# Performance work log

Measured on AMD Instinct MI355X. Metric: run time of the kernel, lower is better.

The kernel has to match this reference:

```python
import jax, jax.numpy as jnp
import numpy as np

B, S, E = 2, 2048, 1024
H, D = 16, 64          # num_heads, head_dim
FF = 4096              # ff_dim = 4*E
EPS = 1e-5


def _layer_norm(x, g, b):
    mu = jnp.mean(x, axis=-1, keepdims=True)
    var = jnp.mean(jnp.square(x - mu), axis=-1, keepdims=True)
    return (x - mu) * jax.lax.rsqrt(var + EPS) * g + b


def setup_inputs() -> dict:
    key = jax.random.key(0)
    ks = jax.random.split(key, 9)
    s = lambda fan_in: 1.0 / np.sqrt(fan_in)
    return {
        "x": jax.random.normal(ks[0], (B, S, E), dtype=jnp.float32),
        "w_qkv": jax.random.uniform(ks[1], (3 * E, E), jnp.float32, -s(E), s(E)),
        "b_qkv": jnp.zeros((3 * E,), jnp.float32),
        "w_out": jax.random.uniform(ks[2], (E, E), jnp.float32, -s(E), s(E)),
        "b_out": jnp.zeros((E,), jnp.float32),
        "g1": jnp.ones((E,), jnp.float32),
        "beta1": jnp.zeros((E,), jnp.float32),
        "w_fc1": jax.random.uniform(ks[3], (FF, E), jnp.float32, -s(E), s(E)),
        "b_fc1": jnp.zeros((FF,), jnp.float32),
        "w_fc2": jax.random.uniform(ks[4], (E, FF), jnp.float32, -s(FF), s(FF)),
        "b_fc2": jnp.zeros((E,), jnp.float32),
        "g2": jnp.ones((E,), jnp.float32),
        "beta2": jnp.zeros((E,), jnp.float32),
    }


def reference(x, w_qkv, b_qkv, w_out, b_out, g1, beta1, w_fc1, b_fc1, w_fc2, b_fc2, g2, beta2):
    scale = 1.0 / np.sqrt(D)
    # QKV projection: [B,S,3E] -> [3,B,H,S,D]
    qkv = (x @ w_qkv.T + b_qkv).reshape(B, S, 3, H, D).transpose(2, 0, 3, 1, 4)
    q, k, v = qkv[0], qkv[1], qkv[2]
    attn = jax.nn.softmax(jnp.einsum('bhqd,bhkd->bhqk', q, k) * scale, axis=-1)
    out = jnp.einsum('bhqk,bhkd->bhqd', attn, v)          # [B,H,S,D]
    out = out.transpose(0, 2, 1, 3).reshape(B, S, E)
    attn_out = out @ w_out.T + b_out
    x1 = _layer_norm(x + attn_out, g1, beta1)
    h = jax.nn.gelu(x1 @ w_fc1.T + b_fc1, approximate=False)  # torch GELU = exact erf
    ff_out = h @ w_fc2.T + b_fc2
    return _layer_norm(x1 + ff_out, g2, beta2)
```

## Files before the change

kernel.cpp:

```cpp
#include <hip/hip_runtime.h>
#include <hip/hip_bf16.h>
#include <math.h>
#include <type_traits>

typedef __hip_bfloat16 bf16;
using short8  = __attribute__((ext_vector_type(8))) short;
using short4v = __attribute__((ext_vector_type(4))) short;
using f32x4   = __attribute__((ext_vector_type(4))) float;

#define TS 2048
#define TH 16
#define TD 64
#define TE 1024
#define T2E 2048

__device__ __forceinline__ void gload16(void* lds, const void* g) {
    __builtin_amdgcn_global_load_lds(
        (__attribute__((address_space(1))) void*)g,
        (__attribute__((address_space(3))) void*)lds, 16, 0, 0);
}

__device__ __forceinline__ uint32_t pktrunc(float a, float b) {
    return (__builtin_bit_cast(uint32_t, a) >> 16) |
           (__builtin_bit_cast(uint32_t, b) & 0xFFFF0000u);
}

__global__ __launch_bounds__(256) void f2b_multi(
    const float* __restrict__ s0, bf16* __restrict__ d0,
    const float* __restrict__ s1, bf16* __restrict__ d1,
    const float* __restrict__ s2, bf16* __restrict__ d2,
    const float* __restrict__ s3, bf16* __restrict__ d3,
    const float* __restrict__ s4, bf16* __restrict__ d4)
{
    int blk = blockIdx.x;
    const float* s; bf16* d; int base;
    if (blk < 2048)      { s = s0; d = d0; base = 0; }
    else if (blk < 3584) { s = s1; d = d1; base = 2048; }
    else if (blk < 4096) { s = s2; d = d2; base = 3584; }
    else if (blk < 6144) { s = s3; d = d3; base = 4096; }
    else                 { s = s4; d = d4; base = 6144; }
    size_t i = ((size_t)(blk - base) * 256 + threadIdx.x) * 8;
    float4 a = *(const float4*)&s[i];
    float4 b = *(const float4*)&s[i + 4];
    bf16 t[8];
    t[0] = __float2bfloat16(a.x); t[1] = __float2bfloat16(a.y);
    t[2] = __float2bfloat16(a.z); t[3] = __float2bfloat16(a.w);
    t[4] = __float2bfloat16(b.x); t[5] = __float2bfloat16(b.y);
    t[6] = __float2bfloat16(b.z); t[7] = __float2bfloat16(b.w);
    *(uint4*)&d[i] = *(uint4*)t;
}

template <typename TC, bool GELU, bool QS, bool WVT, int BN>
__global__ __launch_bounds__(512, 2) void gemm256(
    const bf16* __restrict__ A, const bf16* __restrict__ Bw,
    const float* __restrict__ bias, TC* __restrict__ C,
    bf16* __restrict__ vTout, int M, int N, int K, int kLen, int Cstride)
{
    constexpr int NB = BN / 64;
    constexpr int NI = BN / 64;
    constexpr int WN = BN / 4;
    __shared__ bf16 As[2][256 * 64];
    __shared__ bf16 Bs[2][BN * 64];

    const int t    = threadIdx.x;
    const int lane = t & 63;
    const int wv   = t >> 6;
    const int wr   = wv >> 2;
    const int wc   = wv & 3;
    const int lr   = lane & 15;
    const int lq   = lane >> 4;

    const int gx  = gridDim.x, gxy = gridDim.x * gridDim.y;
    const int nwg = gxy * gridDim.z;
    const int id  = blockIdx.x + gx * blockIdx.y + gxy * blockIdx.z;
    const int sid = (id & 7) * (nwg >> 3) + (id >> 3);
    const int zIdx  = sid / gxy;
    const int rem   = sid - zIdx * gxy;
    const int tm    = rem / gx;
    const int mBase = tm * 256;
    const int nBase = (rem - tm * gx) * BN;
    const int kOff  = zIdx * kLen;

    const int sr = t >> 3;
    const int sc = (t & 7) * 8;
    const int NT = kLen >> 6;

    const bf16* aPt = A  + (size_t)(mBase + sr) * K + sc;
    const bf16* bPt = Bw + (size_t)(nBase + sr) * K + sc;

    f32x4 acc[8][NI];
    #pragma unroll
    for (int mi = 0; mi < 8; mi++)
        #pragma unroll
        for (int ni = 0; ni < NI; ni++)
            acc[mi][ni] = (f32x4){0.f, 0.f, 0.f, 0.f};

    auto stage = [&](int b, int k0) {
        #pragma unroll
        for (int i = 0; i < 4; i++)
            gload16(&As[b][i * 4096 + wv * 512],
                    aPt + (size_t)(i * 64) * K + k0);
        #pragma unroll
        for (int i = 0; i < NB; i++)
            gload16(&Bs[b][i * 4096 + wv * 512],
                    bPt + (size_t)(i * 64) * K + k0);
    };

    stage(0, kOff);
    for (int kt = 0; kt < NT; ++kt) {
        const int cur = kt & 1;
        if (kt + 1 < NT) {
            stage(cur ^ 1, kOff + (kt + 1) * 64);
            if constexpr (BN == 256)
                asm volatile("s_waitcnt vmcnt(8)" ::: "memory");
            else
                asm volatile("s_waitcnt vmcnt(6)" ::: "memory");
        } else {
            asm volatile("s_waitcnt vmcnt(0)" ::: "memory");
        }
        __builtin_amdgcn_s_barrier();
        asm volatile("" ::: "memory");

        short8 bfr[NI][2];
        #pragma unroll
        for (int ni = 0; ni < NI; ni++)
            #pragma unroll
            for (int ks = 0; ks < 2; ks++)
                bfr[ni][ks] = *(const short8*)
                    &Bs[cur][(wc * WN + ni * 16 + lr) * 64 + ks * 32 + lq * 8];
        #pragma unroll
        for (int mi = 0; mi < 8; mi++) {
            short8 a0 = *(const short8*)
                &As[cur][(wr * 128 + mi * 16 + lr) * 64 + lq * 8];
            short8 a1 = *(const short8*)
                &As[cur][(wr * 128 + mi * 16 + lr) * 64 + 32 + lq * 8];
            #pragma unroll
            for (int ni = 0; ni < NI; ni++) {
                acc[mi][ni] = __builtin_amdgcn_mfma_f32_16x16x32_bf16(
                    a0, bfr[ni][0], acc[mi][ni], 0, 0, 0);
                acc[mi][ni] = __builtin_amdgcn_mfma_f32_16x16x32_bf16(
                    a1, bfr[ni][1], acc[mi][ni], 0, 0, 0);
            }
        }
        asm volatile("" ::: "memory");
        __builtin_amdgcn_s_barrier();
    }

    const size_t cOff = (size_t)zIdx * M * Cstride;
    #pragma unroll
    for (int mi = 0; mi < 8; mi++) {
        #pragma unroll
        for (int ni = 0; ni < NI; ni++) {
            int cc = nBase + wc * WN + ni * 16 + lr;
            float bv = (zIdx == 0) ? bias[cc] : 0.f;
            int r0 = mBase + wr * 128 + mi * 16 + lq * 4;
            bool vpath = false;
            if constexpr (WVT) {
                if (cc >= 2 * TE) {
                    vpath = true;
                    int d  = cc - 2 * TE;
                    int s0 = r0 & (TS - 1);
                    int bb = r0 >> 11;
                    int pos = (s0 & ~31) | (((s0 >> 2) & 3) << 3)
                            | (((s0 >> 4) & 1) << 2);
                    bf16 ob[4];
                    #pragma unroll
                    for (int i = 0; i < 4; i++)
                        ob[i] = __float2bfloat16(acc[mi][ni][i] + bv);
                    *(uint2*)&vTout[((size_t)(bb * TH + (d >> 6)) * TD + (d & 63))
                                    * TS + pos] = *(uint2*)ob;
                }
            }
            if (!vpath) {
                #pragma unroll
                for (int i = 0; i < 4; i++) {
                    float v = acc[mi][ni][i] + bv;
                    if constexpr (GELU)
                        v = 0.5f * v * (1.0f + erff(v * 0.70710678118f));
                    if constexpr (QS)
                        if (cc < TE) v *= 0.180336880111f;
                    if constexpr (std::is_same_v<TC, bf16>)
                        C[cOff + (size_t)(r0 + i) * Cstride + cc] = __float2bfloat16(v);
                    else
                        C[cOff + (size_t)(r0 + i) * Cstride + cc] = v;
                }
            }
        }
    }
}

__global__ __launch_bounds__(256, 4) void attn_flash(
    const bf16* __restrict__ qkv, const bf16* __restrict__ vT,
    bf16* __restrict__ attnO)
{
    __shared__ bf16 Ks[128 * 72];
    __shared__ bf16 Vt[64 * 136];

    const int t    = threadIdx.x;
    const int lane = t & 63;
    const int wv   = t >> 6;
    const int c    = lane & 15;
    const int u    = lane >> 4;
    const int bid  = blockIdx.x;
    const int bh   = (bid & 7) * 4 + ((bid >> 3) & 3);
    const int qt   = bid >> 5;
    const int h = bh & 15, b = bh >> 4;
    const size_t tokBase = (size_t)b * TS;
    const int qrow = qt * 64 + wv * 16 + c;

    short8 qf[2];
    #pragma unroll
    for (int kc = 0; kc < 2; kc++)
        qf[kc] = *(const short8*)&qkv[(tokBase + qrow) * T2E + h * TD + kc * 32 + u * 8];

    f32x4 oacc[4];
    #pragma unroll
    for (int di = 0; di < 4; di++) oacc[di] = (f32x4){0.f, 0.f, 0.f, 0.f};
    float lsum = 0.f;

    const int vd = t >> 2;
    const int vc = (t & 3) * 8;
    const bf16* vbase = &vT[((size_t)bh * TD + vd) * TS + vc];

    for (int it = 0; it < 16; it++) {
        const int kb0 = it * 128;
        __syncthreads();

        #pragma unroll
        for (int i = 0; i < 4; i++) {
            int l = t + i * 256;
            int r = l >> 3, ch = (l & 7) * 8;
            *(uint4*)&Ks[r * 72 + ch] =
                *(const uint4*)&qkv[(tokBase + kb0 + r) * T2E + TE + h * TD + ch];
        }
        #pragma unroll
        for (int i = 0; i < 4; i++)
            *(uint4*)&Vt[vd * 136 + vc + i * 32] = *(const uint4*)&vbase[kb0 + i * 32];
        __syncthreads();

        f32x4 sacc[8];
        #pragma unroll
        for (int kc = 0; kc < 2; kc++) {
            #pragma unroll
            for (int kb = 0; kb < 8; kb++) {
                short8 kf = *(const short8*)&Ks[(kb * 16 + c) * 72 + kc * 32 + u * 8];
                sacc[kb] = __builtin_amdgcn_mfma_f32_16x16x32_bf16(
                    kf, qf[kc],
                    kc == 0 ? (f32x4){0.f, 0.f, 0.f, 0.f} : sacc[kb], 0, 0, 0);
            }
        }

        #pragma unroll
        for (int p = 0; p < 4; p++) {
            union { uint32_t d[2]; short4v s; } pb0, pb1;
            {
                float a0 = exp2f(sacc[2*p][0]);
                float a1 = exp2f(sacc[2*p][1]);
                float a2 = exp2f(sacc[2*p][2]);
                float a3 = exp2f(sacc[2*p][3]);
                float b0 = exp2f(sacc[2*p+1][0]);
                float b1 = exp2f(sacc[2*p+1][1]);
                float b2 = exp2f(sacc[2*p+1][2]);
                float b3 = exp2f(sacc[2*p+1][3]);
                lsum += (a0 + a1) + (a2 + a3) + (b0 + b1) + (b2 + b3);
                pb0.d[0] = pktrunc(a0, a1); pb0.d[1] = pktrunc(a2, a3);
                pb1.d[0] = pktrunc(b0, b1); pb1.d[1] = pktrunc(b2, b3);
            }
            #pragma unroll
            for (int di = 0; di < 4; di++) {
                short8 vv = *(const short8*)&Vt[(di * 16 + c) * 136 + p * 32 + u * 8];
                short4v lo = __builtin_shufflevector(vv, vv, 0, 1, 2, 3);
                short4v hi = __builtin_shufflevector(vv, vv, 4, 5, 6, 7);
                oacc[di] = __builtin_amdgcn_mfma_f32_16x16x16bf16_1k(
                    lo, pb0.s, oacc[di], 0, 0, 0);
                oacc[di] = __builtin_amdgcn_mfma_f32_16x16x16bf16_1k(
                    hi, pb1.s, oacc[di], 0, 0, 0);
            }
        }
    }

    lsum += __shfl_xor(lsum, 16, 64);
    lsum += __shfl_xor(lsum, 32, 64);
    const float inv = 1.0f / lsum;

    #pragma unroll
    for (int di = 0; di < 4; di++) {
        bf16 ob[4];
        #pragma unroll
        for (int rg = 0; rg < 4; rg++)
            ob[rg] = __float2bfloat16(oacc[di][rg] * inv);
        *(uint2*)&attnO[(tokBase + qrow) * TE + h * TD + di * 16 + u * 4] = *(uint2*)ob;
    }
}

__global__ __launch_bounds__(256) void add_ln3(
    const float* __restrict__ a, const float* __restrict__ p0,
    const float* __restrict__ p1, const float* __restrict__ g,
    const float* __restrict__ beta, float* __restrict__ out,
    bf16* __restrict__ outb)
{
    __shared__ float r1[256], r2[256];
    const int t = threadIdx.x;
    const size_t row = (size_t)blockIdx.x * TE;

    float4 va = *(const float4*)&a[row + t * 4];
    float4 v0 = *(const float4*)&p0[row + t * 4];
    float4 v1 = *(const float4*)&p1[row + t * 4];
    float v[4] = {va.x + v0.x + v1.x, va.y + v0.y + v1.y,
                  va.z + v0.z + v1.z, va.w + v0.w + v1.w};
    float s = 0.f, s2 = 0.f;
    #pragma unroll
    for (int i = 0; i < 4; i++) { s += v[i]; s2 += v[i] * v[i]; }
    r1[t] = s; r2[t] = s2;
    __syncthreads();
    for (int off = 128; off > 0; off >>= 1) {
        if (t < off) { r1[t] += r1[t + off]; r2[t] += r2[t + off]; }
        __syncthreads();
    }
    const float mu  = r1[0] * (1.f / 1024.f);
    const float var = r2[0] * (1.f / 1024.f) - mu * mu;
    const float rs  = rsqrtf(var + 1e-5f);
    float4 vg  = *(const float4*)&g[t * 4];
    float4 vbt = *(const float4*)&beta[t * 4];
    float o[4];
    o[0] = (v[0] - mu) * rs * vg.x + vbt.x;
    o[1] = (v[1] - mu) * rs * vg.y + vbt.y;
    o[2] = (v[2] - mu) * rs * vg.z + vbt.z;
    o[3] = (v[3] - mu) * rs * vg.w + vbt.w;
    *(float4*)&out[row + t * 4] = *(float4*)o;
    if (outb) {
        bf16 ob[4];
        #pragma unroll
        for (int i = 0; i < 4; i++) ob[i] = __float2bfloat16(o[i]);
        *(uint2*)&outb[row + t * 4] = *(uint2*)ob;
    }
}

extern "C" void kernel_launch(void* const* d_in, const int* in_sizes, int n_in,
                              void* d_out, int out_size, void* d_ws, size_t ws_size,
                              hipStream_t stream)
{
    const float* x     = (const float*)d_in[0];
    const float* w_qkv = (const float*)d_in[1];
    const float* b_qkv = (const float*)d_in[2];
    const float* w_out = (const float*)d_in[3];
    const float* b_out = (const float*)d_in[4];
    const float* g1    = (const float*)d_in[5];
    const float* beta1 = (const float*)d_in[6];
    const float* w_fc1 = (const float*)d_in[7];
    const float* b_fc1 = (const float*)d_in[8];
    const float* w_fc2 = (const float*)d_in[9];
    const float* b_fc2 = (const float*)d_in[10];
    const float* g2    = (const float*)d_in[11];
    const float* beta2 = (const float*)d_in[12];
    float* out = (float*)d_out;

    char* wsb   = (char*)d_ws;
    bf16*  qk    = (bf16*)(wsb);
    bf16*  vT    = (bf16*)(wsb + 16777216);
    bf16*  xb    = (bf16*)(wsb + 25165824);
    float* y     = (float*)(wsb);
    float* ff    = (float*)(wsb);
    bf16*  attnO = (bf16*)(wsb + 33554432);
    bf16*  x1b   = (bf16*)(wsb + 33554432);
    bf16*  wfc1b = (bf16*)(wsb + 41943040);
    bf16*  woutb = (bf16*)(wsb + 50331648);
    bf16*  wqkvb = (bf16*)(wsb + 52428800);
    float* x1    = (float*)(wsb + 67108864);
    bf16*  hbuf  = (bf16*)(wsb + 83886080);
    bf16*  wfc2b = (bf16*)(wsb + 117440512);

    const int M = 2 * TS;
    const size_t PART = (size_t)M * TE;
    dim3 blk(256), blk5(512);

    f2b_multi<<<dim3(8192), blk, 0, stream>>>(
        x, xb, w_qkv, wqkvb, w_out, woutb, w_fc1, wfc1b, w_fc2, wfc2b);

    gemm256<bf16, false, true, true, 256><<<dim3(12, 16, 1), blk5, 0, stream>>>(
        xb, wqkvb, b_qkv, qk, vT, M, 3072, TE, TE, T2E);
    attn_flash<<<dim3(1024), blk, 0, stream>>>(qk, vT, attnO);
    gemm256<float, false, false, false, 128><<<dim3(8, 16, 2), blk5, 0, stream>>>(
        attnO, woutb, b_out, y, nullptr, M, TE, TE, TE / 2, TE);
    add_ln3<<<dim3(M), blk, 0, stream>>>(x, y, y + PART, g1, beta1, x1, x1b);
    gemm256<bf16, true, false, false, 256><<<dim3(16, 16, 1), blk5, 0, stream>>>(
        x1b, wfc1b, b_fc1, hbuf, nullptr, M, 4096, TE, TE, 4096);
    gemm256<float, false, false, false, 128><<<dim3(8, 16, 2), blk5, 0, stream>>>(
        hbuf, wfc2b, b_fc2, ff, nullptr, M, TE, 4096, 2048, TE);
    add_ln3<<<dim3(M), blk, 0, stream>>>(x1, ff, ff + PART, g2, beta2, out, nullptr);
}
```

Baseline: 411.2 us.

## Rework GEMM main loop into 8-phase pipeline with swizzled LDS and priority hints

The GEMM kernel's K loop now handles 128 columns per iteration, split into eight phases. Each phase loads a quarter of the A/B fragments and issues a batch of MFMAs. Global-to-LDS loads for the next half-tiles are interleaved at specific phases, and the LDS layout uses an XOR swizzle to avoid bank conflicts on fragment reads. s_setprio is raised around the MFMA bursts. The aim is to overlap memory and compute more finely and cut LDS bank conflicts. In exchange there are many more barriers per iteration and a hand-tuned vmcnt schedule that must exactly match the number of outstanding loads.

```diff
diff --git a/kernel.cpp b/kernel.cpp
--- a/kernel.cpp
+++ b/kernel.cpp
@@ -51,16 +51,17 @@
 }
 
 template <typename TC, bool GELU, bool QS, bool WVT, int BN>
-__global__ __launch_bounds__(512, 2) void gemm256(
+__global__ __launch_bounds__(512, 2) void gemm8p(
     const bf16* __restrict__ A, const bf16* __restrict__ Bw,
     const float* __restrict__ bias, TC* __restrict__ C,
     bf16* __restrict__ vTout, int M, int N, int K, int kLen, int Cstride)
 {
-    constexpr int NB = BN / 64;
-    constexpr int NI = BN / 64;
-    constexpr int WN = BN / 4;
-    __shared__ bf16 As[2][256 * 64];
-    __shared__ bf16 Bs[2][BN * 64];
+    constexpr int NI    = BN / 64;
+    constexpr int NIP   = NI / 2;
+    constexpr int WN    = BN / 4;
+    constexpr int BHALF = BN * 32;
+    __shared__ bf16 As[2][2 * 8192];
+    __shared__ bf16 Bs[2][2 * BHALF];
 
     const int t    = threadIdx.x;
     const int lane = t & 63;
@@ -82,8 +83,7 @@
     const int kOff  = zIdx * kLen;
 
     const int sr = t >> 3;
-    const int sc = (t & 7) * 8;
-    const int NT = kLen >> 6;
+    const int sc = (((t & 7) ^ ((t >> 3) & 7)) * 8);
 
     const bf16* aPt = A  + (size_t)(mBase + sr) * K + sc;
     const bf16* bPt = Bw + (size_t)(nBase + sr) * K + sc;
@@ -95,55 +95,82 @@
         for (int ni = 0; ni < NI; ni++)
             acc[mi][ni] = (f32x4){0.f, 0.f, 0.f, 0.f};
 
-    auto stage = [&](int b, int k0) {
-        #pragma unroll
-        for (int i = 0; i < 4; i++)
-            gload16(&As[b][i * 4096 + wv * 512],
-                    aPt + (size_t)(i * 64) * K + k0);
-        #pragma unroll
-        for (int i = 0; i < NB; i++)
-            gload16(&Bs[b][i * 4096 + wv * 512],
-                    bPt + (size_t)(i * 64) * K + k0);
+    auto stA = [&](int par, int kcol) {
+        #pragma unroll
+        for (int g = 0; g < 4; g++)
+            gload16(&As[par][g * 4096 + wv * 512],
+                    aPt + (size_t)(g * 64) * K + kcol);
     };
-
-    stage(0, kOff);
-    for (int kt = 0; kt < NT; ++kt) {
-        const int cur = kt & 1;
-        if (kt + 1 < NT) {
-            stage(cur ^ 1, kOff + (kt + 1) * 64);
-            if constexpr (BN == 256)
-                asm volatile("s_waitcnt vmcnt(8)" ::: "memory");
-            else
-                asm volatile("s_waitcnt vmcnt(6)" ::: "memory");
-        } else {
-            asm volatile("s_waitcnt vmcnt(0)" ::: "memory");
+    auto stB = [&](int par, int kcol) {
+        #pragma unroll
+        for (int g = 0; g < BN / 64; g++)
+            gload16(&Bs[par][g * 4096 + wv * 512],
+                    bPt + (size_t)(g * 64) * K + kcol);
+    };
+
+    const int T = kLen >> 7;
+
+    stA(0, kOff); stB(0, kOff); stA(1, kOff + 64);
+    asm volatile("s_waitcnt vmcnt(4)" ::: "memory");
+    __builtin_amdgcn_s_barrier();
+
+    for (int it = 0; it < T; ++it) {
+        const bool more = (it + 1 < T);
+        const int kb = kOff + it * 128;
+        short8 af[4][2];
+        short8 bfv[NIP][2];
+        #pragma unroll
+        for (int p = 0; p < 8; ++p) {
+            const int par = p >> 2;
+            const int mh  = (p >> 1) & 1;
+            const int nq  = p & 1;
+            if (nq == 0) {
+                #pragma unroll
+                for (int m = 0; m < 4; m++)
+                    #pragma unroll
+                    for (int ks = 0; ks < 2; ks++)
+                        af[m][ks] = *(const short8*)&As[par][wr * 8192
+                            + (mh * 64 + m * 16 + lr) * 64
+                            + (((ks * 4 + lq) ^ (lr & 7)) * 8)];
+            }
+            #pragma unroll
+            for (int n = 0; n < NIP; n++)
+                #pragma unroll
+                for (int ks = 0; ks < 2; ks++)
+                    bfv[n][ks] = *(const short8*)&Bs[par][(wc >> 1) * BHALF
+                        + ((wc & 1) * WN + (nq * NIP + n) * 16 + lr) * 64
+                        + (((ks * 4 + lq) ^ (lr & 7)) * 8)];
+            if (p == 0)         stB(1, kb + 64);
+            if (p == 3 && more) stA(0, kb + 128);
+            if (p == 4 && more) stB(0, kb + 128);
+            if (p == 7 && more) stA(1, kb + 192);
+            if (p == 3) {
+                if (more) asm volatile("s_waitcnt vmcnt(4)" ::: "memory");
+                else      asm volatile("s_waitcnt vmcnt(0)" ::: "memory");
+            }
+            if (p == 7 && more) asm volatile("s_waitcnt vmcnt(4)" ::: "memory");
+            asm volatile("" ::: "memory");
+            __builtin_amdgcn_s_barrier();
+            asm volatile("s_waitcnt lgkmcnt(0)" ::: "memory");
+            __builtin_amdgcn_sched_barrier(0);
+            __builtin_amdgcn_s_setprio(1);
+            #pragma unroll
+            for (int m = 0; m < 4; m++)
+                #pragma unroll
+                for (int n = 0; n < NIP; n++) {
+                    acc[mh * 4 + m][nq * NIP + n] =
+                        __builtin_amdgcn_mfma_f32_16x16x32_bf16(
+                            af[m][0], bfv[n][0],
+                            acc[mh * 4 + m][nq * NIP + n], 0, 0, 0);
+                    acc[mh * 4 + m][nq * NIP + n] =
+                        __builtin_amdgcn_mfma_f32_16x16x32_bf16(
+                            af[m][1], bfv[n][1],
+                            acc[mh * 4 + m][nq * NIP + n], 0, 0, 0);
+                }
+            __builtin_amdgcn_s_setprio(0);
+            asm volatile("" ::: "memory");
+            __builtin_amdgcn_s_barrier();
         }
-        __builtin_amdgcn_s_barrier();
-        asm volatile("" ::: "memory");
-
-        short8 bfr[NI][2];
-        #pragma unroll
-        for (int ni = 0; ni < NI; ni++)
-            #pragma unroll
-            for (int ks = 0; ks < 2; ks++)
-                bfr[ni][ks] = *(const short8*)
-                    &Bs[cur][(wc * WN + ni * 16 + lr) * 64 + ks * 32 + lq * 8];
-        #pragma unroll
-        for (int mi = 0; mi < 8; mi++) {
-            short8 a0 = *(const short8*)
-                &As[cur][(wr * 128 + mi * 16 + lr) * 64 + lq * 8];
-            short8 a1 = *(const short8*)
-                &As[cur][(wr * 128 + mi * 16 + lr) * 64 + 32 + lq * 8];
-            #pragma unroll
-            for (int ni = 0; ni < NI; ni++) {
-                acc[mi][ni] = __builtin_amdgcn_mfma_f32_16x16x32_bf16(
-                    a0, bfr[ni][0], acc[mi][ni], 0, 0, 0);
-                acc[mi][ni] = __builtin_amdgcn_mfma_f32_16x16x32_bf16(
-                    a1, bfr[ni][1], acc[mi][ni], 0, 0, 0);
-            }
-        }
-        asm volatile("" ::: "memory");
-        __builtin_amdgcn_s_barrier();
     }
 
     const size_t cOff = (size_t)zIdx * M * Cstride;
@@ -372,20 +399,20 @@
 
     const int M = 2 * TS;
     const size_t PART = (size_t)M * TE;
-    dim3 blk(256), blk5(512);
+    dim3 blk(256), blk8(512);
 
     f2b_multi<<<dim3(8192), blk, 0, stream>>>(
         x, xb, w_qkv, wqkvb, w_out, woutb, w_fc1, wfc1b, w_fc2, wfc2b);
 
-    gemm256<bf16, false, true, true, 256><<<dim3(12, 16, 1), blk5, 0, stream>>>(
+    gemm8p<bf16, false, true, true, 256><<<dim3(12, 16, 1), blk8, 0, stream>>>(
         xb, wqkvb, b_qkv, qk, vT, M, 3072, TE, TE, T2E);
     attn_flash<<<dim3(1024), blk, 0, stream>>>(qk, vT, attnO);
-    gemm256<float, false, false, false, 128><<<dim3(8, 16, 2), blk5, 0, stream>>>(
+    gemm8p<float, false, false, false, 128><<<dim3(8, 16, 2), blk8, 0, stream>>>(
         attnO, woutb, b_out, y, nullptr, M, TE, TE, TE / 2, TE);
     add_ln3<<<dim3(M), blk, 0, stream>>>(x, y, y + PART, g1, beta1, x1, x1b);
-    gemm256<bf16, true, false, false, 256><<<dim3(16, 16, 1), blk5, 0, stream>>>(
+    gemm8p<bf16, true, false, false, 256><<<dim3(16, 16, 1), blk8, 0, stream>>>(
         x1b, wfc1b, b_fc1, hbuf, nullptr, M, 4096, TE, TE, 4096);
-    gemm256<float, false, false, false, 128><<<dim3(8, 16, 2), blk5, 0, stream>>>(
+    gemm8p<float, false, false, false, 128><<<dim3(8, 16, 2), blk8, 0, stream>>>(
         hbuf, wfc2b, b_fc2, ff, nullptr, M, TE, 4096, 2048, TE);
     add_ln3<<<dim3(M), blk, 0, stream>>>(x1, ff, ff + PART, g2, beta2, out, nullptr);
 }
```

Measured after the change: 454.0 us. 10.4% more time.
